# Kernel tuning notes

Hardware: AMD Instinct MI355X
Metric: run time of the kernel (lower is better)

Reference implementation:

```python
import jax, jax.numpy as jnp
import numpy as np

B, S, D, K = 8, 2048, 1024, 204  # K = int(0.1 * seq_len)
LN_EPS = 1e-12


def setup_inputs() -> dict:
    key = jax.random.key(0)
    ks = jax.random.split(key, 8)
    scale = 0.02
    return {
        "input_tensor": jax.random.normal(ks[0], (B, S, D), jnp.float32),
        "attention_mask": jnp.zeros((B, 1, 1, S), jnp.float32),  # unused by module
        "Wq": jax.random.normal(ks[1], (D, K), jnp.float32) * scale,
        "bq": jnp.zeros((K,), jnp.float32),
        "Wk": jax.random.normal(ks[2], (D, K), jnp.float32) * scale,
        "bk": jnp.zeros((K,), jnp.float32),
        "Wv": jax.random.normal(ks[3], (D, D), jnp.float32) * scale,
        "bv": jnp.zeros((D,), jnp.float32),
        "Wd": jax.random.normal(ks[4], (D, D), jnp.float32) * scale,
        "bd": jnp.zeros((D,), jnp.float32),
        "gamma": jnp.ones((D,), jnp.float32),
        "beta": jnp.zeros((D,), jnp.float32),
    }


def reference(input_tensor, attention_mask, Wq, bq, Wk, bk, Wv, bv, Wd, bd, gamma, beta):
    # factorized synthesizer: low-rank (k=204) Q/K projections
    q = input_tensor @ Wq + bq          # [B,S,K]
    k = input_tensor @ Wk + bk          # [B,S,K]
    v = input_tensor @ Wv + bv          # [B,S,D]
    scores = jnp.einsum('bsk,btk->bst', q, k)          # [B,S,S]
    probs = jax.nn.softmax(scores, axis=-1)
    # per-head matmul with broadcast probs == direct matmul on merged heads
    ctx = jnp.einsum('bst,btd->bsd', probs, v)          # [B,S,D]
    h = ctx @ Wd + bd
    y = h + input_tensor                                 # residual
    mean = jnp.mean(y, axis=-1, keepdims=True)
    var = jnp.mean(jnp.square(y - mean), axis=-1, keepdims=True)
    return gamma * (y - mean) / jnp.sqrt(var + LN_EPS) + beta
```

## Files before the change

kernel.cpp:

```cpp
#include <hip/hip_runtime.h>
#include <stdint.h>

#define BB 8
#define SS 2048
#define DD 1024
#define KREAL 204

typedef __attribute__((ext_vector_type(8))) short short8;
typedef __attribute__((ext_vector_type(4))) float floatx4;
typedef uint16_t u16;
typedef uint32_t u32;

__device__ __forceinline__ float bf2f(u16 u) {
    union { float f; u32 i; } c; c.i = ((u32)u) << 16; return c.f;
}
__device__ __forceinline__ u16 f2bf(float f) {
    union { float f; u32 i; } c; c.f = f;
    u32 i = c.i;
    u32 r = (i + 0x7FFFu + ((i >> 16) & 1u)) >> 16;
    return (u16)r;
}

#if defined(__has_builtin)
#if __has_builtin(__builtin_amdgcn_global_load_lds)
#define HAVE_GLL 1
#endif
#endif

__device__ __forceinline__ void gload16(const u16* g, u16* l) {
#ifdef HAVE_GLL
    __builtin_amdgcn_global_load_lds(
        (const __attribute__((address_space(1))) void*)(uintptr_t)g,
        (__attribute__((address_space(3))) void*)(u32)(uintptr_t)(void*)l,
        16, 0, 0);
#else
    *(uint4*)l = *(const uint4*)g;
#endif
}

#define VM_WAIT(N) asm volatile("s_waitcnt vmcnt(" #N ")" ::: "memory")
#define S_BAR()    asm volatile("s_barrier" ::: "memory")

__device__ __forceinline__ void stage64(const u16* __restrict__ src, size_t ld,
                                        u16* lds, int tid) {
#pragma unroll
    for (int j = 0; j < 2; j++) {
        int flat = j * 256 + tid;
        int row = flat >> 3, slot = flat & 7;
        int kg = slot ^ (row & 7);
        gload16(src + (size_t)row * ld + kg * 8, lds + flat * 8);
    }
}
__device__ __forceinline__ short8 frag(const u16* lds, int row, int kslot) {
    return *(const short8*)&lds[(row << 6) + (((kslot ^ (row & 7)) & 7) << 3)];
}

__device__ __forceinline__ short8 frag32(const u16* plane, int row, int ks) {
    return *(const short8*)&plane[(row << 5) + (((ks ^ ((row >> 1) & 3)) & 3) << 3)];
}

template <int MT0, bool LOADB>
__device__ __forceinline__ void phase16(const u16* Apl, const u16* Bpl,
                                        int arow, int brow, int ln, int quad,
                                        short8 (&bv)[4], floatx4 (&acc)[8][4]) {
    short8 af[4];
#pragma unroll
    for (int i = 0; i < 4; i++) af[i] = frag32(Apl, arow + (MT0 + i) * 16 + ln, quad);
    if (LOADB) {
#pragma unroll
        for (int nt = 0; nt < 4; nt++) bv[nt] = frag32(Bpl, brow + nt * 16 + ln, quad);
    }
    __builtin_amdgcn_s_setprio(1);
#pragma unroll
    for (int i = 0; i < 4; i++)
#pragma unroll
        for (int nt = 0; nt < 4; nt++)
            acc[MT0 + i][nt] = __builtin_amdgcn_mfma_f32_16x16x32_bf16(
                af[i], bv[nt], acc[MT0 + i][nt], 0, 0, 0);
    __builtin_amdgcn_s_setprio(0);
}

#define RING5_BODY(SHCALL)                                                     \
    short8 bv[4];                                                              \
    int sl0 = 0, sl1 = 1;                                                      \
    _Pragma("unroll 2")                                                        \
    for (int t = 0; t < NT - 2; ++t) {                                         \
        const u16* Ap0 = Al + sl0 * 8192;  const u16* Bp0 = Bl + sl0 * 8192;   \
        const u16* Ap1 = Al + sl1 * 8192;  const u16* Bp1 = Bl + sl1 * 8192;   \
        const int st = sl0 ? sl0 - 1 : 4;                                      \
        VM_WAIT(12); S_BAR();                                                  \
        SHCALL(st, 2 * t + 4);                                                 \
        phase16<0, true >(Ap0, Bp0, arow, brow, ln, quad, bv, acc);            \
        phase16<4, false>(Ap0, Bp0, arow, brow, ln, quad, bv, acc);            \
        VM_WAIT(12); S_BAR();                                                  \
        SHCALL(sl0, 2 * t + 5);                                                \
        phase16<0, true >(Ap1, Bp1, arow, brow, ln, quad, bv, acc);            \
        phase16<4, false>(Ap1, Bp1, arow, brow, ln, quad, bv, acc);            \
        sl0 += 2; if (sl0 >= 5) sl0 -= 5;                                      \
        sl1 += 2; if (sl1 >= 5) sl1 -= 5;                                      \
    }                                                                          \
    {                                                                          \
        const u16* Ap0 = Al + sl0 * 8192;  const u16* Bp0 = Bl + sl0 * 8192;   \
        const u16* Ap1 = Al + sl1 * 8192;  const u16* Bp1 = Bl + sl1 * 8192;   \
        VM_WAIT(12); S_BAR();                                                  \
        phase16<0, true >(Ap0, Bp0, arow, brow, ln, quad, bv, acc);            \
        phase16<4, false>(Ap0, Bp0, arow, brow, ln, quad, bv, acc);            \
        VM_WAIT(8); S_BAR();                                                   \
        phase16<0, true >(Ap1, Bp1, arow, brow, ln, quad, bv, acc);            \
        phase16<4, false>(Ap1, Bp1, arow, brow, ln, quad, bv, acc);            \
        sl0 += 2; if (sl0 >= 5) sl0 -= 5;                                      \
        sl1 += 2; if (sl1 >= 5) sl1 -= 5;                                      \
    }                                                                          \
    {                                                                          \
        const u16* Ap0 = Al + sl0 * 8192;  const u16* Bp0 = Bl + sl0 * 8192;   \
        const u16* Ap1 = Al + sl1 * 8192;  const u16* Bp1 = Bl + sl1 * 8192;   \
        VM_WAIT(4); S_BAR();                                                   \
        phase16<0, true >(Ap0, Bp0, arow, brow, ln, quad, bv, acc);            \
        phase16<4, false>(Ap0, Bp0, arow, brow, ln, quad, bv, acc);            \
        VM_WAIT(0); S_BAR();                                                   \
        phase16<0, true >(Ap1, Bp1, arow, brow, ln, quad, bv, acc);            \
        phase16<4, false>(Ap1, Bp1, arow, brow, ln, quad, bv, acc);            \
    }

template <int NT>
__device__ __forceinline__ void gemm_core5(
    const u16* __restrict__ Ag, size_t lda,
    const u16* __restrict__ Bg, size_t ldb,
    u16* lds, int tid, floatx4 (&acc)[8][4]) {
    static_assert(NT >= 3, "ring-5 core needs NT >= 3");
    const int lane = tid & 63, w = tid >> 6;
    const int arow = (w >> 2) * 128, brow = (w & 3) * 64;
    const int ln = lane & 15, quad = lane >> 4;
    const int srow = tid >> 2;
    const int kgp = (tid & 3) ^ ((srow >> 1) & 3);
    const u16* A0 = Ag + (size_t)srow * lda + kgp * 8;
    const u16* A1 = Ag + (size_t)(srow + 128) * lda + kgp * 8;
    const u16* B0 = Bg + (size_t)srow * ldb + kgp * 8;
    const u16* B1 = Bg + (size_t)(srow + 128) * ldb + kgp * 8;
    u16* Al = lds;
    u16* Bl = lds + 5 * 8192;

    auto SH = [&](int sl, int h) {
        size_t koff = (size_t)h * 32;
        gload16(A0 + koff, Al + sl * 8192 + tid * 8);
        gload16(A1 + koff, Al + sl * 8192 + 4096 + tid * 8);
        gload16(B0 + koff, Bl + sl * 8192 + tid * 8);
        gload16(B1 + koff, Bl + sl * 8192 + 4096 + tid * 8);
    };

    SH(0, 0); SH(1, 1); SH(2, 2); SH(3, 3);
    RING5_BODY(SH)
}

template <int NT>
__device__ __forceinline__ void gemm_core5p(
    const u16* __restrict__ Ag, size_t PSA,
    const u16* __restrict__ Bg, size_t PSB,
    u16* lds, int tid, floatx4 (&acc)[8][4]) {
    static_assert(NT >= 3, "ring-5 core needs NT >= 3");
    const int lane = tid & 63, w = tid >> 6;
    const int arow = (w >> 2) * 128, brow = (w & 3) * 64;
    const int ln = lane & 15, quad = lane >> 4;
    const int srow = tid >> 2;
    const int kgp = (tid & 3) ^ ((srow >> 1) & 3);
    const u16* A0 = Ag + (size_t)srow * 32 + kgp * 8;
    const u16* A1 = A0 + 4096;
    const u16* B0 = Bg + (size_t)srow * 32 + kgp * 8;
    const u16* B1 = B0 + 4096;
    u16* Al = lds;
    u16* Bl = lds + 5 * 8192;

    auto SH = [&](int sl, int h) {
        gload16(A0 + (size_t)h * PSA, Al + sl * 8192 + tid * 8);
        gload16(A1 + (size_t)h * PSA, Al + sl * 8192 + 4096 + tid * 8);
        gload16(B0 + (size_t)h * PSB, Bl + sl * 8192 + tid * 8);
        gload16(B1 + (size_t)h * PSB, Bl + sl * 8192 + 4096 + tid * 8);
    };

    SH(0, 0); SH(1, 1); SH(2, 2); SH(3, 3);
    RING5_BODY(SH)
}

template <typename F>
__device__ __forceinline__ void store_rm256(u16* smem, u16* gbase, size_t ldc,
                                            int wm, int wn, int ln, int quad,
                                            int tid, F val) {
    for (int half = 0; half < 2; half++) {
        __syncthreads();
        if (wm == half) {
#pragma unroll
            for (int mt = 0; mt < 8; mt++)
#pragma unroll
                for (int nt = 0; nt < 4; nt++)
#pragma unroll
                    for (int r = 0; r < 4; r++)
                        smem[(mt * 16 + quad * 4 + r) * 264 + wn * 64 + nt * 16 + ln] =
                            val(mt, nt, r);
        }
        __syncthreads();
#pragma unroll
        for (int j = 0; j < 8; j++) {
            int flat = j * 512 + tid;
            int row = flat >> 5, c = flat & 31;
            *(uint4*)&gbase[(size_t)(half * 128 + row) * ldc + c * 8] =
                *(const uint4*)&smem[row * 264 + c * 8];
        }
    }
}

template <typename F>
__device__ __forceinline__ void store_pm256(u16* smem, u16* pb, int s0, int t0,
                                            int wm, int wn, int ln, int quad,
                                            int tid, F val) {
    for (int half = 0; half < 2; half++) {
        __syncthreads();
        if (wm == half) {
#pragma unroll
            for (int mt = 0; mt < 8; mt++)
#pragma unroll
                for (int nt = 0; nt < 4; nt++)
#pragma unroll
                    for (int r = 0; r < 4; r++)
                        smem[(mt * 16 + quad * 4 + r) * 264 + wn * 64 + nt * 16 + ln] =
                            val(mt, nt, r);
        }
        __syncthreads();
#pragma unroll
        for (int j = 0; j < 8; j++) {
            int flat = j * 512 + tid;
            int row = flat >> 5, c = flat & 31;
            size_t panel = (size_t)(t0 >> 5) + (c >> 2);
            *(uint4*)&pb[panel * 65536 + (size_t)(s0 + half * 128 + row) * 32 + (c & 3) * 8] =
                *(const uint4*)&smem[row * 264 + c * 8];
        }
    }
}

template <typename F4>
__device__ __forceinline__ void store_tr256_pm(u16* smem, u16* utb, int n0,
                                               int s0loc, int wm, int wn,
                                               int ln, int quad, int tid, F4 val4) {
    for (int qr = 0; qr < 4; qr++) {
        __syncthreads();
        if (wn == qr) {
#pragma unroll
            for (int mt = 0; mt < 8; mt++)
#pragma unroll
                for (int nt = 0; nt < 4; nt++) {
                    ushort4 v = val4(mt, nt);
                    *(ushort4*)&smem[(nt * 16 + ln) * 264 + wm * 128 + mt * 16 + quad * 4] = v;
                }
        }
        __syncthreads();
#pragma unroll
        for (int j = 0; j < 4; j++) {
            int flat = j * 512 + tid;
            int c = flat >> 5, r8 = flat & 31;
            size_t panel = (size_t)(s0loc >> 5) + (r8 >> 2);
            *(uint4*)&utb[panel * 32768 + (size_t)(n0 + qr * 64 + c) * 32 + (r8 & 3) * 8] =
                *(const uint4*)&smem[c * 264 + r8 * 8];
        }
    }
}

__global__ __launch_bounds__(256) void k_cast_bf16(
    const float* __restrict__ x, u16* __restrict__ o) {
    size_t i = ((size_t)blockIdx.x * 256 + threadIdx.x) * 4;
    float4 v = *(const float4*)&x[i];
    ushort4 p;
    p.x = f2bf(v.x); p.y = f2bf(v.y); p.z = f2bf(v.z); p.w = f2bf(v.w);
    *(ushort4*)&o[i] = p;
}

__global__ __launch_bounds__(256) void k_prep(
    const float* __restrict__ Wq, const float* __restrict__ Wk,
    const float* __restrict__ Wv, const float* __restrict__ Wd,
    const float* __restrict__ bv, const float* __restrict__ bd,
    const float* __restrict__ bq, const float* __restrict__ bk,
    u16* __restrict__ Wqkt, u16* __restrict__ Wv16, u16* __restrict__ Wdt,
    float* __restrict__ bc, float* __restrict__ bqk) {
    const int z = blockIdx.z;
    const int t = threadIdx.x;
    if (z == 4) {
        int id = blockIdx.y * 32 + blockIdx.x;
        if (id < 16) {
            __shared__ float red[4][64];
            int n = id * 64 + (t & 63);
            int dc = t >> 6;
            float s = 0.f;
            for (int d = dc * 256; d < dc * 256 + 256; d++)
                s += bv[d] * Wd[(size_t)d * 1024 + n];
            red[dc][t & 63] = s;
            __syncthreads();
            if (dc == 0) bc[n] = bd[n] + red[0][t & 63] + red[1][t & 63] + red[2][t & 63] + red[3][t & 63];
        } else if (id == 16) {
            for (int i = t; i < 512; i += 256) {
                float v = 0.f;
                if (i < KREAL) v = bq[i];
                else if (i >= 256 && i < 256 + KREAL) v = bk[i - 256];
                bqk[i] = v;
            }
        }
        return;
    }
    __shared__ u16 tile[32][33];
    int k0 = blockIdx.x * 32, n0 = blockIdx.y * 32;
    int tx = t & 31, ty = t >> 5;
    if (z == 2) {
        for (int i = ty; i < 32; i += 8) {
            size_t idx = (size_t)(k0 + i) * 1024 + n0 + tx;
            Wv16[idx] = f2bf(Wv[idx]);
        }
        return;
    }
    const float* W; u16* out; int N, Npad, rowoff;
    if (z == 0)      { W = Wq; out = Wqkt; N = KREAL; Npad = 256;  rowoff = 0;   }
    else if (z == 1) { W = Wk; out = Wqkt; N = KREAL; Npad = 256;  rowoff = 256; }
    else             { W = Wd; out = Wdt;  N = 1024;  Npad = 1024; rowoff = 0;   }
    if (n0 >= Npad) return;
    for (int i = ty; i < 32; i += 8) {
        int n = n0 + tx;
        tile[i][tx] = (n < N) ? f2bf(W[(size_t)(k0 + i) * N + n]) : (u16)0;
    }
    __syncthreads();
    for (int i = ty; i < 32; i += 8) {
        int n = n0 + i;
        if (n < Npad) out[(size_t)(rowoff + n) * 1024 + k0 + tx] = tile[tx][i];
    }
}

__global__ __launch_bounds__(256) void k_gemm64(
    const u16* __restrict__ A, const u16* __restrict__ Bt,
    u16* __restrict__ C, int ldc) {
    __shared__ u16 As[64 * 64];
    __shared__ u16 Bs[64 * 64];
    const int tid = threadIdx.x;
    const int m0 = blockIdx.x * 64, n0 = blockIdx.y * 64;
    const int lane = tid & 63, w = tid >> 6;
    const int ln = lane & 15, quad = lane >> 4;

    floatx4 acc[4];
    floatx4 zero = {0.f, 0.f, 0.f, 0.f};
#pragma unroll
    for (int nt = 0; nt < 4; nt++) acc[nt] = zero;

    for (int kt = 0; kt < 16; kt++) {
        __syncthreads();
        stage64(A + (size_t)m0 * 1024 + kt * 64, 1024, As, tid);
        stage64(Bt + (size_t)n0 * 1024 + kt * 64, 1024, Bs, tid);
        __syncthreads();
#pragma unroll
        for (int kk = 0; kk < 2; kk++) {
            short8 av = frag(As, w * 16 + ln, kk * 4 + quad);
#pragma unroll
            for (int nt = 0; nt < 4; nt++) {
                short8 bvf = frag(Bs, nt * 16 + ln, kk * 4 + quad);
                acc[nt] = __builtin_amdgcn_mfma_f32_16x16x32_bf16(av, bvf, acc[nt], 0, 0, 0);
            }
        }
    }
    const int row0 = m0 + w * 16 + quad * 4;
#pragma unroll
    for (int nt = 0; nt < 4; nt++) {
        const int col = n0 + nt * 16 + ln;
        ushort4 pk;
        pk.x = f2bf(acc[nt][0]); pk.y = f2bf(acc[nt][1]);
        pk.z = f2bf(acc[nt][2]); pk.w = f2bf(acc[nt][3]);
        *reinterpret_cast<ushort4*>(&C[(size_t)col * ldc + row0]) = pk;
    }
}

__global__ __launch_bounds__(512, 2) void k_proj2(
    const u16* __restrict__ A, const u16* __restrict__ Wqkt,
    const u16* __restrict__ Wvdt, const float* __restrict__ bqk,
    u16* __restrict__ qkp, u16* __restrict__ ut) {
    __shared__ __align__(16) u16 lds[81920];
    const int tid = threadIdx.x;
    const int m0 = blockIdx.x * 256;
    const int by = blockIdx.y;
    const int lane = tid & 63, w = tid >> 6;
    const int wm = w >> 2, wn = w & 3;
    const int ln = lane & 15, quad = lane >> 4;

    floatx4 acc[8][4];
    floatx4 zero = {0.f, 0.f, 0.f, 0.f};
#pragma unroll
    for (int mt = 0; mt < 8; mt++)
#pragma unroll
        for (int nt = 0; nt < 4; nt++) acc[mt][nt] = zero;

    const u16* Ag = A + (size_t)m0 * 1024;
    const int n0 = (by < 2) ? by * 256 : (by - 2) * 256;
    const u16* Bg = (by < 2) ? (Wqkt + (size_t)n0 * 1024) : (Wvdt + (size_t)n0 * 1024);
    gemm_core5<16>(Ag, 1024, Bg, 1024, lds, tid, acc);

    if (by < 2) {
        float b4[4];
#pragma unroll
        for (int nt = 0; nt < 4; nt++) b4[nt] = bqk[n0 + wn * 64 + nt * 16 + ln];
        store_rm256(lds, qkp + (size_t)m0 * 512 + n0, 512, wm, wn, ln, quad, tid,
            [&](int mt, int nt, int r) -> u16 {
                return f2bf(acc[mt][nt][r] + b4[nt]);
            });
    } else {
        int b = m0 >> 11, s0loc = m0 & 2047;
        store_tr256_pm(lds, ut + (size_t)b * DD * SS, n0, s0loc, wm, wn, ln, quad, tid,
            [&](int mt, int nt) -> ushort4 {
                ushort4 pk;
                pk.x = f2bf(acc[mt][nt][0]); pk.y = f2bf(acc[mt][nt][1]);
                pk.z = f2bf(acc[mt][nt][2]); pk.w = f2bf(acc[mt][nt][3]);
                return pk;
            });
    }
}

__global__ __launch_bounds__(512, 2) void k_qk2(
    const u16* __restrict__ qkp, u16* __restrict__ P, float* __restrict__ lg) {
    __shared__ __align__(16) u16 lds[81920];
    const int tid = threadIdx.x;
    const int s0 = blockIdx.x * 256, t0 = blockIdx.y * 256, bb = blockIdx.z;
    const int lane = tid & 63, w = tid >> 6;
    const int wm = w >> 2, wn = w & 3;
    const int ln = lane & 15, quad = lane >> 4;

    floatx4 acc[8][4];
    floatx4 zero = {0.f, 0.f, 0.f, 0.f};
#pragma unroll
    for (int mt = 0; mt < 8; mt++)
#pragma unroll
        for (int nt = 0; nt < 4; nt++) acc[mt][nt] = zero;

    gemm_core5<4>(qkp + ((size_t)bb * SS + s0) * 512, 512,
                  qkp + ((size_t)bb * SS + t0) * 512 + 256, 512, lds, tid, acc);

#pragma unroll
    for (int mt = 0; mt < 8; mt++)
#pragma unroll
        for (int nt = 0; nt < 4; nt++)
#pragma unroll
            for (int r = 0; r < 4; r++)
                acc[mt][nt][r] = __expf(acc[mt][nt][r] - 30.f);

#pragma unroll
    for (int mt = 0; mt < 8; mt++) {
#pragma unroll
        for (int r = 0; r < 4; r++) {
            float rs = acc[mt][0][r] + acc[mt][1][r] + acc[mt][2][r] + acc[mt][3][r];
            rs += __shfl_xor(rs, 1);
            rs += __shfl_xor(rs, 2);
            rs += __shfl_xor(rs, 4);
            rs += __shfl_xor(rs, 8);
            if (ln == 0)
                atomicAdd(&lg[(size_t)bb * SS + s0 + wm * 128 + mt * 16 + quad * 4 + r], rs);
        }
    }

    store_pm256(lds, P + (size_t)bb * SS * SS, s0, t0, wm, wn, ln, quad, tid,
        [&](int mt, int nt, int r) -> u16 { return f2bf(acc[mt][nt][r]); });
}

__global__ __launch_bounds__(512, 2) void k_h2(
    const u16* __restrict__ P, const u16* __restrict__ ut,
    const float* __restrict__ lg, const float* __restrict__ bc,
    const float* __restrict__ xres, float* __restrict__ out) {
    __shared__ __align__(16) u16 lds[81920];
    const int tid = threadIdx.x;
    const int s0 = blockIdx.x * 256, d0 = blockIdx.y * 256, bb = blockIdx.z;
    const int lane = tid & 63, w = tid >> 6;
    const int wm = w >> 2;
    const int ln = lane & 15, quad = lane >> 4;

    floatx4 acc[8][4];
    floatx4 zero = {0.f, 0.f, 0.f, 0.f};
#pragma unroll
    for (int mt = 0; mt < 8; mt++)
#pragma unroll
        for (int nt = 0; nt < 4; nt++) acc[mt][nt] = zero;

    gemm_core5p<32>(P + (size_t)bb * SS * SS + (size_t)s0 * 32, (size_t)SS * 32,
                    ut + (size_t)bb * DD * SS + (size_t)d0 * 32, (size_t)DD * 32,
                    lds, tid, acc);

    float* smem = (float*)lds;
    float* outb = out + ((size_t)bb * SS + s0) * DD + d0;
    const float* xb = xres + ((size_t)bb * SS + s0) * DD + d0;
    const float* lgb = lg + (size_t)bb * SS + s0;
    const int wn = w & 3;
    for (int c4 = 0; c4 < 4; c4++) {
        __syncthreads();
        if (wm == (c4 >> 1)) {
#pragma unroll
            for (int i = 0; i < 4; i++)
#pragma unroll
                for (int nt = 0; nt < 4; nt++)
#pragma unroll
                    for (int r = 0; r < 4; r++)
                        smem[(i * 16 + quad * 4 + r) * 260 + wn * 64 + nt * 16 + ln] =
                            acc[(c4 & 1) * 4 + i][nt][r];
        }
        __syncthreads();
#pragma unroll
        for (int j = 0; j < 8; j++) {
            int flat = j * 512 + tid;
            int row = flat >> 6, q = flat & 63;
            float iv = 1.f / lgb[c4 * 64 + row];
            float4 a  = *(const float4*)&smem[row * 260 + q * 4];
            float4 b4 = *(const float4*)&bc[d0 + q * 4];
            float4 xr = *(const float4*)&xb[(size_t)(c4 * 64 + row) * DD + q * 4];
            float4 o;
            o.x = a.x * iv + b4.x + xr.x;
            o.y = a.y * iv + b4.y + xr.y;
            o.z = a.z * iv + b4.z + xr.z;
            o.w = a.w * iv + b4.w + xr.w;
            *(float4*)&outb[(size_t)(c4 * 64 + row) * DD + q * 4] = o;
        }
    }
}

__global__ __launch_bounds__(256) void k_ln_f32(
    float* __restrict__ io, const float* __restrict__ gamma,
    const float* __restrict__ beta) {
    const int tid = threadIdx.x;
    const int lane = tid & 63, w = tid >> 6;
    const size_t row = (size_t)blockIdx.x * 4 + w;
    float* rp = io + row * DD;

    float v[16];
#pragma unroll
    for (int j = 0; j < 4; j++) {
        float4 t = *(const float4*)&rp[j * 256 + lane * 4];
        v[j * 4 + 0] = t.x; v[j * 4 + 1] = t.y; v[j * 4 + 2] = t.z; v[j * 4 + 3] = t.w;
    }
    float s = 0.f, sq = 0.f;
#pragma unroll
    for (int i = 0; i < 16; i++) { s += v[i]; sq += v[i] * v[i]; }
#pragma unroll
    for (int msk = 1; msk < 64; msk <<= 1) {
        s  += __shfl_xor(s,  msk, 64);
        sq += __shfl_xor(sq, msk, 64);
    }
    float mean = s * (1.f / 1024.f);
    float var  = sq * (1.f / 1024.f) - mean * mean;
    float rstd = rsqrtf(fmaxf(var, 0.f) + 1e-12f);
#pragma unroll
    for (int j = 0; j < 4; j++) {
        float4 g  = *(const float4*)&gamma[j * 256 + lane * 4];
        float4 bt = *(const float4*)&beta [j * 256 + lane * 4];
        float4 o;
        o.x = g.x * (v[j * 4 + 0] - mean) * rstd + bt.x;
        o.y = g.y * (v[j * 4 + 1] - mean) * rstd + bt.y;
        o.z = g.z * (v[j * 4 + 2] - mean) * rstd + bt.z;
        o.w = g.w * (v[j * 4 + 3] - mean) * rstd + bt.w;
        *(float4*)&rp[j * 256 + lane * 4] = o;
    }
}

extern "C" void kernel_launch(void* const* d_in, const int* in_sizes, int n_in,
                              void* d_out, int out_size, void* d_ws, size_t ws_size,
                              hipStream_t stream) {
    const float* x     = (const float*)d_in[0];
    const float* Wq    = (const float*)d_in[2];
    const float* bq    = (const float*)d_in[3];
    const float* Wk    = (const float*)d_in[4];
    const float* bk    = (const float*)d_in[5];
    const float* Wv    = (const float*)d_in[6];
    const float* bv    = (const float*)d_in[7];
    const float* Wd    = (const float*)d_in[8];
    const float* bd    = (const float*)d_in[9];
    const float* gamma = (const float*)d_in[10];
    const float* beta  = (const float*)d_in[11];
    float* out = (float*)d_out;

    char* ws = (char*)d_ws;
    u16*   qkp  = (u16*)(ws + 0);
    u16*   ut   = (u16*)(ws + 16777216);
    u16*   P    = (u16*)(ws + 50331648);
    u16*   x16  = (u16*)(ws + 50331648);
    u16*   Wv16 = (u16*)(ws + 83886080);
    u16*   Wvdt = (u16*)(ws + 85983232);
    u16*   Wdt  = (u16*)(ws + 88080384);
    u16*   Wqkt = (u16*)(ws + 90177536);
    float* lg   = (float*)(ws + 117440512);
    float* bc   = (float*)(ws + 117506048);
    float* bqk  = (float*)(ws + 117510144);

    k_cast_bf16<<<dim3(16384), dim3(256), 0, stream>>>(x, x16);
    k_prep<<<dim3(32, 32, 5), dim3(256), 0, stream>>>(Wq, Wk, Wv, Wd, bv, bd, bq, bk,
                                                      Wqkt, Wv16, Wdt, bc, bqk);
    k_gemm64<<<dim3(16, 16), dim3(256), 0, stream>>>(Wv16, Wdt, Wvdt, 1024);

    k_proj2<<<dim3(64, 6), dim3(512), 0, stream>>>(x16, Wqkt, Wvdt, bqk, qkp, ut);

    hipMemsetAsync(lg, 0, (size_t)BB * SS * sizeof(float), stream);

    k_qk2<<<dim3(8, 8, 8), dim3(512), 0, stream>>>(qkp, P, lg);
    k_h2 <<<dim3(8, 4, 8), dim3(512), 0, stream>>>(P, ut, lg, bc, x, out);

    k_ln_f32<<<dim3(4096), dim3(256), 0, stream>>>(out, gamma, beta);
}
```

Baseline: 367.0 us.

## Stage B operand through registers in ring GEMM and fuse prep launches

The ring-5 GEMM cores now load the B tile into registers two steps ahead and write it to LDS with ordinary stores, while A still uses direct global-to-LDS loads. This halves the outstanding direct-LDS loads per stage and adds lgkmcnt waits before each barrier. Separately, the bf16 cast of x, the weight prep and the zeroing of the logsumexp buffer are merged into one launch, removing a kernel launch and a memset. The register staging adds VGPR pressure and extra LDS store traffic, and the tail of the loop now has fewer barriers.

```diff
diff --git a/kernel.cpp b/kernel.cpp
--- a/kernel.cpp
+++ b/kernel.cpp
@@ -39,6 +39,7 @@
 }
 
 #define VM_WAIT(N) asm volatile("s_waitcnt vmcnt(" #N ")" ::: "memory")
+#define LGKM0()    asm volatile("s_waitcnt lgkmcnt(0)" ::: "memory")
 #define S_BAR()    asm volatile("s_barrier" ::: "memory")
 
 __device__ __forceinline__ void stage64(const u16* __restrict__ src, size_t ld,
@@ -80,7 +81,7 @@
     __builtin_amdgcn_s_setprio(0);
 }
 
-#define RING5_BODY(SHCALL)                                                     \
+#define RING5H_BODY(POINTC)                                                    \
     short8 bv[4];                                                              \
     int sl0 = 0, sl1 = 1;                                                      \
     _Pragma("unroll 2")                                                        \
@@ -88,36 +89,34 @@
         const u16* Ap0 = Al + sl0 * 8192;  const u16* Bp0 = Bl + sl0 * 8192;   \
         const u16* Ap1 = Al + sl1 * 8192;  const u16* Bp1 = Bl + sl1 * 8192;   \
         const int st = sl0 ? sl0 - 1 : 4;                                      \
-        VM_WAIT(12); S_BAR();                                                  \
-        SHCALL(st, 2 * t + 4);                                                 \
+        VM_WAIT(12); LGKM0(); S_BAR();                                         \
+        POINTC(st, 2 * t + 4, 0, 2 * t + 6, (2 * t + 6 < 2 * NT));             \
         phase16<0, true >(Ap0, Bp0, arow, brow, ln, quad, bv, acc);            \
         phase16<4, false>(Ap0, Bp0, arow, brow, ln, quad, bv, acc);            \
-        VM_WAIT(12); S_BAR();                                                  \
-        SHCALL(sl0, 2 * t + 5);                                                \
+        VM_WAIT(12); LGKM0(); S_BAR();                                         \
+        POINTC(sl0, 2 * t + 5, 1, 2 * t + 7, (2 * t + 7 < 2 * NT));            \
         phase16<0, true >(Ap1, Bp1, arow, brow, ln, quad, bv, acc);            \
         phase16<4, false>(Ap1, Bp1, arow, brow, ln, quad, bv, acc);            \
         sl0 += 2; if (sl0 >= 5) sl0 -= 5;                                      \
         sl1 += 2; if (sl1 >= 5) sl1 -= 5;                                      \
     }                                                                          \
-    {                                                                          \
+    {             \
         const u16* Ap0 = Al + sl0 * 8192;  const u16* Bp0 = Bl + sl0 * 8192;   \
         const u16* Ap1 = Al + sl1 * 8192;  const u16* Bp1 = Bl + sl1 * 8192;   \
-        VM_WAIT(12); S_BAR();                                                  \
+        VM_WAIT(4); LGKM0(); S_BAR();                                          \
         phase16<0, true >(Ap0, Bp0, arow, brow, ln, quad, bv, acc);            \
         phase16<4, false>(Ap0, Bp0, arow, brow, ln, quad, bv, acc);            \
-        VM_WAIT(8); S_BAR();                                                   \
         phase16<0, true >(Ap1, Bp1, arow, brow, ln, quad, bv, acc);            \
         phase16<4, false>(Ap1, Bp1, arow, brow, ln, quad, bv, acc);            \
         sl0 += 2; if (sl0 >= 5) sl0 -= 5;                                      \
         sl1 += 2; if (sl1 >= 5) sl1 -= 5;                                      \
     }                                                                          \
-    {                                                                          \
+    {                                                            \
         const u16* Ap0 = Al + sl0 * 8192;  const u16* Bp0 = Bl + sl0 * 8192;   \
         const u16* Ap1 = Al + sl1 * 8192;  const u16* Bp1 = Bl + sl1 * 8192;   \
-        VM_WAIT(4); S_BAR();                                                   \
+        VM_WAIT(0); LGKM0(); S_BAR();                                          \
         phase16<0, true >(Ap0, Bp0, arow, brow, ln, quad, bv, acc);            \
         phase16<4, false>(Ap0, Bp0, arow, brow, ln, quad, bv, acc);            \
-        VM_WAIT(0); S_BAR();                                                   \
         phase16<0, true >(Ap1, Bp1, arow, brow, ln, quad, bv, acc);            \
         phase16<4, false>(Ap1, Bp1, arow, brow, ln, quad, bv, acc);            \
     }
@@ -140,16 +139,28 @@
     u16* Al = lds;
     u16* Bl = lds + 5 * 8192;
 
-    auto SH = [&](int sl, int h) {
-        size_t koff = (size_t)h * 32;
-        gload16(A0 + koff, Al + sl * 8192 + tid * 8);
-        gload16(A1 + koff, Al + sl * 8192 + 4096 + tid * 8);
-        gload16(B0 + koff, Bl + sl * 8192 + tid * 8);
-        gload16(B1 + koff, Bl + sl * 8192 + 4096 + tid * 8);
-    };
-
-    SH(0, 0); SH(1, 1); SH(2, 2); SH(3, 3);
-    RING5_BODY(SH)
+    uint4 rb[2][2];
+#define LD_B(dst, h)                                                           \
+    { dst[0] = *(const uint4*)(B0 + (size_t)(h) * 32);                         \
+      dst[1] = *(const uint4*)(B1 + (size_t)(h) * 32); }
+#define POINTR(sl, h, par, hload, doload)                                      \
+    {                                                                          \
+        *(uint4*)(Bl + (sl) * 8192 + tid * 8)        = rb[par][0];             \
+        *(uint4*)(Bl + (sl) * 8192 + 4096 + tid * 8) = rb[par][1];             \
+        gload16(A0 + (size_t)(h) * 32, Al + (sl) * 8192 + tid * 8);            \
+        gload16(A1 + (size_t)(h) * 32, Al + (sl) * 8192 + 4096 + tid * 8);     \
+        if (doload) LD_B(rb[par], hload);                                      \
+    }
+
+    LD_B(rb[0], 0); LD_B(rb[1], 1);
+    POINTR(0, 0, 0, 2, true);
+    POINTR(1, 1, 1, 3, true);
+    POINTR(2, 2, 0, 4, true);
+    POINTR(3, 3, 1, 5, true);
+
+    RING5H_BODY(POINTR)
+#undef POINTR
+#undef LD_B
 }
 
 template <int NT>
@@ -170,15 +181,28 @@
     u16* Al = lds;
     u16* Bl = lds + 5 * 8192;
 
-    auto SH = [&](int sl, int h) {
-        gload16(A0 + (size_t)h * PSA, Al + sl * 8192 + tid * 8);
-        gload16(A1 + (size_t)h * PSA, Al + sl * 8192 + 4096 + tid * 8);
-        gload16(B0 + (size_t)h * PSB, Bl + sl * 8192 + tid * 8);
-        gload16(B1 + (size_t)h * PSB, Bl + sl * 8192 + 4096 + tid * 8);
-    };
-
-    SH(0, 0); SH(1, 1); SH(2, 2); SH(3, 3);
-    RING5_BODY(SH)
+    uint4 rb[2][2];
+#define LD_B(dst, h)                                                           \
+    { dst[0] = *(const uint4*)(B0 + (size_t)(h) * PSB);                        \
+      dst[1] = *(const uint4*)(B1 + (size_t)(h) * PSB); }
+#define POINTP(sl, h, par, hload, doload)                                      \
+    {                                                                          \
+        *(uint4*)(Bl + (sl) * 8192 + tid * 8)        = rb[par][0];             \
+        *(uint4*)(Bl + (sl) * 8192 + 4096 + tid * 8) = rb[par][1];             \
+        gload16(A0 + (size_t)(h) * PSA, Al + (sl) * 8192 + tid * 8);           \
+        gload16(A1 + (size_t)(h) * PSA, Al + (sl) * 8192 + 4096 + tid * 8);    \
+        if (doload) LD_B(rb[par], hload);                                      \
+    }
+
+    LD_B(rb[0], 0); LD_B(rb[1], 1);
+    POINTP(0, 0, 0, 2, true);
+    POINTP(1, 1, 1, 3, true);
+    POINTP(2, 2, 0, 4, true);
+    POINTP(3, 3, 1, 5, true);
+
+    RING5H_BODY(POINTP)
+#undef POINTP
+#undef LD_B
 }
 
 template <typename F>
@@ -263,24 +287,28 @@
     }
 }
 
-__global__ __launch_bounds__(256) void k_cast_bf16(
-    const float* __restrict__ x, u16* __restrict__ o) {
-    size_t i = ((size_t)blockIdx.x * 256 + threadIdx.x) * 4;
-    float4 v = *(const float4*)&x[i];
-    ushort4 p;
-    p.x = f2bf(v.x); p.y = f2bf(v.y); p.z = f2bf(v.z); p.w = f2bf(v.w);
-    *(ushort4*)&o[i] = p;
-}
-
-__global__ __launch_bounds__(256) void k_prep(
+__global__ __launch_bounds__(256) void k_prepall(
+    const float* __restrict__ x, u16* __restrict__ x16,
     const float* __restrict__ Wq, const float* __restrict__ Wk,
     const float* __restrict__ Wv, const float* __restrict__ Wd,
     const float* __restrict__ bv, const float* __restrict__ bd,
     const float* __restrict__ bq, const float* __restrict__ bk,
     u16* __restrict__ Wqkt, u16* __restrict__ Wv16, u16* __restrict__ Wdt,
-    float* __restrict__ bc, float* __restrict__ bqk) {
+    float* __restrict__ bc, float* __restrict__ bqk, float* __restrict__ lg) {
     const int z = blockIdx.z;
     const int t = threadIdx.x;
+    if (z == 5) {
+        int id = blockIdx.y * 32 + blockIdx.x;
+#pragma unroll
+        for (int j = 0; j < 16; j++) {
+            size_t i = ((size_t)j * 262144 + (size_t)id * 256 + t) * 4;
+            float4 v = *(const float4*)&x[i];
+            ushort4 p;
+            p.x = f2bf(v.x); p.y = f2bf(v.y); p.z = f2bf(v.z); p.w = f2bf(v.w);
+            *(ushort4*)&x16[i] = p;
+        }
+        return;
+    }
     if (z == 4) {
         int id = blockIdx.y * 32 + blockIdx.x;
         if (id < 16) {
@@ -300,6 +328,9 @@
                 else if (i >= 256 && i < 256 + KREAL) v = bk[i - 256];
                 bqk[i] = v;
             }
+        } else if (id < 25) {
+            int seg = id - 17;
+            for (int i = t; i < 2048; i += 256) lg[seg * 2048 + i] = 0.f;
         }
         return;
     }
@@ -584,14 +615,11 @@
     float* bc   = (float*)(ws + 117506048);
     float* bqk  = (float*)(ws + 117510144);
 
-    k_cast_bf16<<<dim3(16384), dim3(256), 0, stream>>>(x, x16);
-    k_prep<<<dim3(32, 32, 5), dim3(256), 0, stream>>>(Wq, Wk, Wv, Wd, bv, bd, bq, bk,
-                                                      Wqkt, Wv16, Wdt, bc, bqk);
+    k_prepall<<<dim3(32, 32, 6), dim3(256), 0, stream>>>(
+        x, x16, Wq, Wk, Wv, Wd, bv, bd, bq, bk, Wqkt, Wv16, Wdt, bc, bqk, lg);
     k_gemm64<<<dim3(16, 16), dim3(256), 0, stream>>>(Wv16, Wdt, Wvdt, 1024);
 
     k_proj2<<<dim3(64, 6), dim3(512), 0, stream>>>(x16, Wqkt, Wvdt, bqk, qkp, ut);
-
-    hipMemsetAsync(lg, 0, (size_t)BB * SS * sizeof(float), stream);
 
     k_qk2<<<dim3(8, 8, 8), dim3(512), 0, stream>>>(qkp, P, lg);
     k_h2 <<<dim3(8, 4, 8), dim3(512), 0, stream>>>(P, ut, lg, bc, x, out);
```

New measurement: 439.7 us. +19.8%, slower.
